# Performance work log

Measured on AMD Instinct MI355X. Metric: run time of the kernel, lower is better.

## Reference

```python
import jax, jax.numpy as jnp
import numpy as np

B, C, H, W = 4, 256, 64, 64
C8 = C // 8

def setup_inputs() -> dict:
    key = jax.random.key(0)
    ks = jax.random.split(key, 9)
    s_in = 1.0 / np.sqrt(C)
    return {
        "feat1": jax.random.normal(ks[0], (B, C, H, W), jnp.float32),
        "feat2": jax.random.normal(ks[1], (B, C, H, W), jnp.float32),
        # 1x1 conv weights stored as [out_ch, in_ch]
        "Wq": jax.random.normal(ks[2], (C8, C), jnp.float32) * s_in,
        "bq": jax.random.normal(ks[3], (C8,), jnp.float32) * s_in,
        "Wk": jax.random.normal(ks[4], (C8, C), jnp.float32) * s_in,
        "bk": jax.random.normal(ks[5], (C8,), jnp.float32) * s_in,
        "Wv": jax.random.normal(ks[6], (C, C), jnp.float32) * s_in,
        "bv": jax.random.normal(ks[7], (C,), jnp.float32) * s_in,
        "gamma": jax.random.normal(ks[8], (1,), jnp.float32) * 0.1,
    }

def reference(feat1, feat2, Wq, bq, Wk, bk, Wv, bv, gamma):
    b, c, h, w = feat1.shape
    n = h * w
    f1 = feat1.reshape(b, c, n)  # [B,C,N]
    f2 = feat2.reshape(b, c, n)
    # 1x1 convs == per-pixel channel matmuls
    q = jnp.einsum("oc,bcn->bno", Wq, f1) + bq            # [B,N,C8]
    k = jnp.einsum("oc,bcn->bon", Wk, f2) + bk[None, :, None]  # [B,C8,N]
    v = jnp.einsum("oc,bcn->bon", Wv, f2) + bv[None, :, None]  # [B,C,N]
    energy = jnp.einsum("bno,bom->bnm", q, k)             # [B,N,N] (unscaled)
    attn = jax.nn.softmax(energy, axis=-1)
    # out[b,c,m] = sum_n v[b,c,n] * attn[b,m,n]
    out = jnp.einsum("bcn,bmn->bcm", v, attn).reshape(b, c, h, w)
    return gamma * out + feat1
```

## Files before the change

### kernel.cpp

```cpp
#include <hip/hip_runtime.h>
#include <hip/hip_bf16.h>
#include <stdint.h>

typedef __attribute__((ext_vector_type(8))) short bf16x8;
typedef __attribute__((ext_vector_type(4))) short short4v;
typedef __attribute__((ext_vector_type(4))) float f32x4;
typedef __attribute__((ext_vector_type(16))) float f32x16;
typedef __attribute__((ext_vector_type(4))) unsigned uint4v;

#define LDS3(p) ((__attribute__((address_space(3))) void*)(p))
#define GLB1(p) ((const __attribute__((address_space(1))) void*)(p))

constexpr int Bc = 4;
constexpr int Cc = 256;
constexpr int Nn = 4096;
constexpr int Dq = 32;
constexpr float L2E = 1.4426950408889634f;

__device__ __forceinline__ short f2b(float x) {
  union { float f; uint32_t u; } v; v.f = x;
  uint32_t r = (v.u + 0x7fffu + ((v.u >> 16) & 1u)) >> 16;
  return (short)(r & 0xffffu);
}
__device__ __forceinline__ float b2f(short s) {
  union { uint32_t u; float f; } v; v.u = ((uint32_t)(uint16_t)s) << 16;
  return v.f;
}
__device__ __forceinline__ unsigned fb(float x) {
  union { float f; unsigned u; } v; v.f = x; return v.u;
}

__global__ __launch_bounds__(256) void prep_transpose(
    const float* __restrict__ f1, const float* __restrict__ f2,
    short* __restrict__ f1T, short* __restrict__ f2T) {
  __shared__ float tile[64][65];
  const int bx = blockIdx.x;
  const int which = bx >> 10;
  const int rem = bx & 1023;
  const int b = rem >> 8;
  const int cb = (rem >> 6) & 3;
  const int nb = rem & 63;
  const float* src = which ? f2 : f1;
  short* dst = which ? f2T : f1T;
  const int c0 = cb * 64, n0 = nb * 64;
  const int tid = threadIdx.x;
  const int lane = tid & 63;
  const int row4 = tid >> 6;
#pragma unroll
  for (int i = 0; i < 16; ++i) {
    const int cl = row4 + i * 4;
    tile[cl][lane] = src[(size_t)(b * Cc + c0 + cl) * Nn + n0 + lane];
  }
  __syncthreads();
#pragma unroll
  for (int i = 0; i < 16; ++i) {
    const int nl = row4 + i * 4;
    dst[(size_t)(b * Nn + n0 + nl) * Cc + c0 + lane] = f2b(tile[lane][nl]);
  }
}

__global__ __launch_bounds__(256) void prep_weights(
    const float* __restrict__ Wq, const float* __restrict__ Wk,
    const float* __restrict__ Wv, short* __restrict__ Wq_b,
    short* __restrict__ Wk_b, short* __restrict__ Wv_b) {
  const int base = (blockIdx.x * 256 + threadIdx.x) * 4;
#pragma unroll
  for (int j = 0; j < 4; ++j) {
    const int idx = base + j;
    if (idx < 8192) Wq_b[idx] = f2b(Wq[idx]);
    else if (idx < 16384) Wk_b[idx - 8192] = f2b(Wk[idx - 8192]);
    else if (idx < 16384 + 65536) Wv_b[idx - 16384] = f2b(Wv[idx - 16384]);
  }
}

__global__ __launch_bounds__(256) void proj_qkv(
    const short* __restrict__ f1T, const short* __restrict__ f2T,
    const short* __restrict__ Wq_b, const float* __restrict__ bq,
    const short* __restrict__ Wk_b, const float* __restrict__ bk,
    const short* __restrict__ Wv_b, const float* __restrict__ bv,
    short* __restrict__ q_ws, short* __restrict__ k_ws,
    short* __restrict__ v_ws) {
  const int bx = blockIdx.x;
  const int b = bx >> 6;
  const int n0 = (bx & 63) * 64;
  const int tid = threadIdx.x;
  const int w = tid >> 6;
  const int lane = tid & 63;
  const int l16 = lane & 15;
  const int g = lane >> 4;

#pragma unroll
  for (int qk = 0; qk < 2; ++qk) {
    const short* X = qk ? f2T : f1T;
    const short* Wm = qk ? Wk_b : Wq_b;
    const float* bias_p = qk ? bk : bq;
    short* outp = qk ? k_ws : q_ws;
    f32x4 accq[2] = {(f32x4){0.f, 0.f, 0.f, 0.f}, (f32x4){0.f, 0.f, 0.f, 0.f}};
#pragma unroll
    for (int kc = 0; kc < 8; ++kc) {
      const bf16x8 a = *(const bf16x8*)&X[(size_t)(b * Nn + n0 + w * 16 + l16) * Cc + kc * 32 + g * 8];
#pragma unroll
      for (int ob = 0; ob < 2; ++ob) {
        const bf16x8 bb = *(const bf16x8*)&Wm[(ob * 16 + l16) * Cc + kc * 32 + g * 8];
        accq[ob] = __builtin_amdgcn_mfma_f32_16x16x32_bf16(a, bb, accq[ob], 0, 0, 0);
      }
    }
#pragma unroll
    for (int ob = 0; ob < 2; ++ob) {
      const float bias = bias_p[ob * 16 + l16];
#pragma unroll
      for (int r = 0; r < 4; ++r) {
        const int n = n0 + w * 16 + g * 4 + r;
        outp[(size_t)(b * Nn + n) * Dq + ob * 16 + l16] = f2b(accq[ob][r] + bias);
      }
    }
  }

  {
    f32x4 acc[4][4];
#pragma unroll
    for (int ci = 0; ci < 4; ++ci)
#pragma unroll
      for (int nb = 0; nb < 4; ++nb) acc[ci][nb] = (f32x4){0.f, 0.f, 0.f, 0.f};
#pragma unroll
    for (int kc = 0; kc < 8; ++kc) {
      bf16x8 bfr[4];
#pragma unroll
      for (int nb = 0; nb < 4; ++nb)
        bfr[nb] = *(const bf16x8*)&f2T[(size_t)(b * Nn + n0 + nb * 16 + l16) * Cc + kc * 32 + g * 8];
#pragma unroll
      for (int ci = 0; ci < 4; ++ci) {
        const bf16x8 afr = *(const bf16x8*)&Wv_b[((w * 4 + ci) * 16 + l16) * Cc + kc * 32 + g * 8];
#pragma unroll
        for (int nb = 0; nb < 4; ++nb)
          acc[ci][nb] = __builtin_amdgcn_mfma_f32_16x16x32_bf16(afr, bfr[nb], acc[ci][nb], 0, 0, 0);
      }
    }
#pragma unroll
    for (int ci = 0; ci < 4; ++ci) {
#pragma unroll
      for (int r = 0; r < 4; ++r) {
        const int c = (w * 4 + ci) * 16 + g * 4 + r;
        const float bias = bv[c];
#pragma unroll
        for (int nb = 0; nb < 4; ++nb) {
          const int n = n0 + nb * 16 + l16;
          v_ws[(size_t)(b * Cc + c) * Nn + n] = f2b(acc[ci][nb][r] + bias);
        }
      }
    }
  }
}

constexpr int NT = 64;
constexpr int VBUF = 256 * NT * 2;
constexpr int SBYTES = 2 * VBUF;

template <int KS>
__global__ __launch_bounds__(256, 2) void attn_kernel(
    const short* __restrict__ q_ws, const short* __restrict__ k_ws,
    const short* __restrict__ v_ws, short* __restrict__ Opart,
    float* __restrict__ mlm, short* __restrict__ mll) {
  constexpr int KSPAN = Nn / KS;
  constexpr int NTILES = KSPAN / NT;
  __shared__ __align__(16) char smem[SBYTES];
  const int bx = blockIdx.x;
  const int swz = (bx & 7) * (16 * KS) + (bx >> 3);
  const int ks = swz >> 7;
  const int rem = swz & 127;
  const int b = rem >> 5;
  const int m0 = (rem & 31) * 128;
  const int n0 = ks * KSPAN;
  const int tid = threadIdx.x;
  const int w = tid >> 6;
  const int lane = tid & 63;
  const int l31 = lane & 31;
  const int h = lane >> 5;

  const short* qbase = q_ws + (size_t)(b * Nn + m0 + w * 32 + l31) * Dq + h * 8;
  const bf16x8 qf0 = *(const bf16x8*)(qbase);
  const bf16x8 qf1 = *(const bf16x8*)(qbase + 16);

  const int kswap = (l31 & 0x13) | ((l31 & 4) << 1) | ((l31 & 8) >> 1);
  const short* kptr = k_ws + (size_t)(b * Nn + n0 + kswap) * Dq + h * 8;

  const int cth = tid >> 3;
  const int c7 = cth & 7;
  const int koff = 8 * ((tid & 7) ^ c7);
  const short* vsrc[8];
#pragma unroll
  for (int j = 0; j < 8; ++j)
    vsrc[j] = v_ws + (size_t)(b * Cc + j * 32 + cth) * Nn + n0 + koff;

  f32x16 acc[8] = {};
  float mrun = -INFINITY, lrun = 0.f;

#pragma unroll
  for (int j = 0; j < 8; ++j) {
    char* ldst = &smem[(j * 256 + tid) * 16];
    __builtin_amdgcn_global_load_lds(GLB1(vsrc[j]), LDS3(ldst), 16, 0, 0);
    vsrc[j] += NT;
  }
  bf16x8 kf[4];
#pragma unroll
  for (int nb = 0; nb < 2; ++nb)
#pragma unroll
    for (int s = 0; s < 2; ++s)
      kf[nb * 2 + s] = *(const bf16x8*)(kptr + nb * 32 * Dq + s * 16);
  kptr += NT * Dq;

  const f32x16 Z = {};
  for (int t = 0; t < NTILES; ++t) {
    const int buf = t & 1;
    f32x16 sa[2];
    sa[0] = __builtin_amdgcn_mfma_f32_32x32x16_bf16(kf[0], qf0, Z, 0, 0, 0);
    sa[0] = __builtin_amdgcn_mfma_f32_32x32x16_bf16(kf[1], qf1, sa[0], 0, 0, 0);
    sa[1] = __builtin_amdgcn_mfma_f32_32x32x16_bf16(kf[2], qf0, Z, 0, 0, 0);
    sa[1] = __builtin_amdgcn_mfma_f32_32x32x16_bf16(kf[3], qf1, sa[1], 0, 0, 0);

    float tmax = sa[0][0];
#pragma unroll
    for (int r = 1; r < 16; ++r) tmax = fmaxf(tmax, sa[0][r]);
#pragma unroll
    for (int r = 0; r < 16; ++r) tmax = fmaxf(tmax, sa[1][r]);
    tmax = fmaxf(tmax, __shfl_xor(tmax, 32));
    if (__any(tmax > mrun + 8.f)) {
      const float mnew = fmaxf(mrun, tmax);
      const float scl = exp2f((mrun - mnew) * L2E);
      float sv[16];
#pragma unroll
      for (int r = 0; r < 16; ++r)
        sv[r] = __shfl(scl, (r & 3) + 8 * (r >> 2) + 4 * h);
#pragma unroll
      for (int cb = 0; cb < 8; ++cb)
#pragma unroll
        for (int r = 0; r < 16; ++r) acc[cb][r] *= sv[r];
      lrun *= scl;
      mrun = mnew;
    }
    const float nml = -mrun * L2E;
    float psum = 0.f;
    unsigned pu[16];
#pragma unroll
    for (int nb = 0; nb < 2; ++nb)
#pragma unroll
      for (int q = 0; q < 8; ++q) {
        const float p0 = exp2f(fmaf(sa[nb][2 * q], L2E, nml));
        const float p1 = exp2f(fmaf(sa[nb][2 * q + 1], L2E, nml));
        psum += p0 + p1;
        pu[nb * 8 + q] = __builtin_amdgcn_perm(fb(p1), fb(p0), 0x07060302u);
      }
    psum += __shfl_xor(psum, 32);
    lrun += psum;

    asm volatile("s_waitcnt vmcnt(0)" ::: "memory");
    __syncthreads();

    if (t + 1 < NTILES) {
#pragma unroll
      for (int j = 0; j < 8; ++j) {
        char* ldst = &smem[(buf ^ 1) * VBUF + (j * 256 + tid) * 16];
        __builtin_amdgcn_global_load_lds(GLB1(vsrc[j]), LDS3(ldst), 16, 0, 0);
        vsrc[j] += NT;
      }
#pragma unroll
      for (int nb = 0; nb < 2; ++nb)
#pragma unroll
        for (int s = 0; s < 2; ++s)
          kf[nb * 2 + s] = *(const bf16x8*)(kptr + nb * 32 * Dq + s * 16);
      kptr += NT * Dq;
    }

    const int sb = buf * VBUF;
#pragma unroll
    for (int f = 0; f < 4; ++f) {
      const uint4v au = {pu[4 * f], pu[4 * f + 1], pu[4 * f + 2], pu[4 * f + 3]};
      const bf16x8 A = __builtin_bit_cast(bf16x8, au);
      const char* vbase =
          &smem[sb + l31 * 128 + ((((f << 1) + h) ^ (l31 & 7)) << 4)];
#pragma unroll
      for (int cb = 0; cb < 8; ++cb) {
        const bf16x8 vB = *(const bf16x8*)(vbase + cb * 4096);
        acc[cb] = __builtin_amdgcn_mfma_f32_32x32x16_bf16(A, vB, acc[cb], 0, 0, 0);
      }
    }
  }

  __syncthreads();
  if (h == 0) {
    const int m = m0 + w * 32 + l31;
    mlm[(size_t)(ks * Bc + b) * Nn + m] = mrun;
    mll[(size_t)(ks * Bc + b) * Nn + m] = f2b(lrun);
  }
  char* strip = smem + w * 10240;
#pragma unroll
  for (int ph = 0; ph < 2; ++ph) {
#pragma unroll
    for (int cb2 = 0; cb2 < 4; ++cb2) {
      const int cb = ph * 4 + cb2;
      const int cs = cb2 * 32 + l31;
#pragma unroll
      for (int q = 0; q < 8; ++q) {
        const int mloc = ((2 * q) & 3) + 8 * (q >> 1) + 4 * h;
        const unsigned pv = __builtin_amdgcn_perm(
            fb(acc[cb][2 * q + 1]), fb(acc[cb][2 * q]), 0x07060302u);
        *(unsigned*)(strip + cs * 80 + mloc * 2) = pv;
      }
    }
    asm volatile("s_waitcnt lgkmcnt(0)" ::: "memory");
#pragma unroll
    for (int i = 0; i < 8; ++i) {
      const int gi = i * 64 + lane;
      const int cs = gi >> 2, gq = gi & 3;
      const uint4v vv = *(const uint4v*)(strip + cs * 80 + gq * 16);
      const int cg = ph * 128 + cs;
      const size_t off =
          ((size_t)(ks * Bc + b) * Cc + cg) * Nn + m0 + w * 32 + gq * 8;
      *(uint4v*)&Opart[off] = vv;
    }
    asm volatile("s_waitcnt lgkmcnt(0)" ::: "memory");
  }
}

template <int KS>
__global__ __launch_bounds__(256) void combine_kernel(
    const short* __restrict__ Opart, const float* __restrict__ mlm,
    const short* __restrict__ mll, const float* __restrict__ feat1,
    const float* __restrict__ gamma_p, float* __restrict__ out) {
  __shared__ float aLDS[KS][64];
  const int bx = blockIdx.x;
  const int b = bx >> 6;
  const int m0 = (bx & 63) * 64;
  const int tid = threadIdx.x;
  if (tid < 64) {
    const int m = m0 + tid;
    float mm[KS], ll[KS], ms = -INFINITY;
#pragma unroll
    for (int ks = 0; ks < KS; ++ks) {
      mm[ks] = mlm[(size_t)(ks * Bc + b) * Nn + m];
      ll[ks] = b2f(mll[(size_t)(ks * Bc + b) * Nn + m]);
      ms = fmaxf(ms, mm[ks]);
    }
    float es[KS], lsum = 0.f;
#pragma unroll
    for (int ks = 0; ks < KS; ++ks) {
      es[ks] = exp2f((mm[ks] - ms) * L2E);
      lsum += ll[ks] * es[ks];
    }
    const float inv = 1.f / lsum;
#pragma unroll
    for (int ks = 0; ks < KS; ++ks) aLDS[ks][tid] = es[ks] * inv;
  }
  __syncthreads();
  const int mg = tid & 7;
  const int cb = tid >> 3;
  float aks[KS][8];
#pragma unroll
  for (int ks = 0; ks < KS; ++ks)
#pragma unroll
    for (int j = 0; j < 8; ++j) aks[ks][j] = aLDS[ks][mg * 8 + j];
  const float gam = gamma_p[0];
#pragma unroll 2
  for (int i = 0; i < 8; ++i) {
    const int c = cb + i * 32;
    float v[8] = {0.f, 0.f, 0.f, 0.f, 0.f, 0.f, 0.f, 0.f};
#pragma unroll
    for (int ks = 0; ks < KS; ++ks) {
      const bf16x8 ov = *(const bf16x8*)
          &Opart[((size_t)(ks * Bc + b) * Cc + c) * Nn + m0 + mg * 8];
#pragma unroll
      for (int j = 0; j < 8; ++j) v[j] += b2f(ov[j]) * aks[ks][j];
    }
    const size_t base = ((size_t)(b * Cc + c)) * Nn + m0 + mg * 8;
    const f32x4 fa = *(const f32x4*)&feat1[base];
    const f32x4 fbv = *(const f32x4*)&feat1[base + 4];
    f32x4 o0, o1;
#pragma unroll
    for (int j = 0; j < 4; ++j) {
      o0[j] = gam * v[j] + fa[j];
      o1[j] = gam * v[4 + j] + fbv[j];
    }
    *(f32x4*)&out[base] = o0;
    *(f32x4*)&out[base + 4] = o1;
  }
}

extern "C" void kernel_launch(void* const* d_in, const int* in_sizes, int n_in,
                              void* d_out, int out_size, void* d_ws,
                              size_t ws_size, hipStream_t stream) {
  const float* feat1 = (const float*)d_in[0];
  const float* feat2 = (const float*)d_in[1];
  const float* Wq = (const float*)d_in[2];
  const float* bq = (const float*)d_in[3];
  const float* Wk = (const float*)d_in[4];
  const float* bk = (const float*)d_in[5];
  const float* Wv = (const float*)d_in[6];
  const float* bv = (const float*)d_in[7];
  const float* gamma = (const float*)d_in[8];
  float* out = (float*)d_out;
  char* ws = (char*)d_ws;

  const size_t need4 = 44433408;
  if (ws_size >= need4) {
    short* Opart = (short*)(ws + 0);
    short* f1T  = (short*)(ws + 0);
    short* f2T  = (short*)(ws + 8388608);
    short* Wq_b = (short*)(ws + 16777216);
    short* Wk_b = (short*)(ws + 16793600);
    short* Wv_b = (short*)(ws + 16809984);
    short* q_ws = (short*)(ws + 33554432);
    short* k_ws = (short*)(ws + 34603008);
    short* v_ws = (short*)(ws + 35651584);
    float* mlm  = (float*)(ws + 44040192);
    short* mll  = (short*)(ws + 44302336);

    prep_transpose<<<2048, 256, 0, stream>>>(feat1, feat2, f1T, f2T);
    prep_weights<<<80, 256, 0, stream>>>(Wq, Wk, Wv, Wq_b, Wk_b, Wv_b);
    proj_qkv<<<256, 256, 0, stream>>>(f1T, f2T, Wq_b, bq, Wk_b, bk, Wv_b, bv,
                                      q_ws, k_ws, v_ws);
    attn_kernel<4><<<512, 256, 0, stream>>>(q_ws, k_ws, v_ws, Opart, mlm, mll);
    combine_kernel<4><<<256, 256, 0, stream>>>(Opart, mlm, mll, feat1, gamma,
                                               out);
  } else {
    short* Opart = (short*)(ws + 0);
    short* f1T  = (short*)(ws + 0);
    short* f2T  = (short*)(ws + 8388608);
    short* Wq_b = (short*)(ws + 16777216);
    short* Wk_b = (short*)(ws + 16793600);
    short* Wv_b = (short*)(ws + 16809984);
    short* q_ws = (short*)(ws + 16941056);
    short* k_ws = (short*)(ws + 17989632);
    short* v_ws = (short*)(ws + 19038208);
    float* mlm  = (float*)(ws + 27426816);
    short* mll  = (short*)(ws + 27557888);

    prep_transpose<<<2048, 256, 0, stream>>>(feat1, feat2, f1T, f2T);
    prep_weights<<<80, 256, 0, stream>>>(Wq, Wk, Wv, Wq_b, Wk_b, Wv_b);
    proj_qkv<<<256, 256, 0, stream>>>(f1T, f2T, Wq_b, bq, Wk_b, bk, Wv_b, bv,
                                      q_ws, k_ws, v_ws);
    attn_kernel<2><<<256, 256, 0, stream>>>(q_ws, k_ws, v_ws, Opart, mlm, mll);
    combine_kernel<2><<<256, 256, 0, stream>>>(Opart, mlm, mll, feat1, gamma,
                                               out);
  }
}
```

Measured before the change: 102.6 us.

## Software-pipeline attention: compute next tile's softmax while current PV MFMAs run

Shrinks the key tile from 64 to 32 and restructures the flash-attention loop so that the QK scores and softmax probabilities for tile t+1 are computed before the PV MFMAs for tile t, with a prologue for the first tile. Deferred rescaling of the accumulators, s_setprio around the MFMA block, and tree reductions for max/sum are added. The V LDS staging layout and the epilogue strip sizes are adjusted to the smaller tile. The aim is to overlap exp/VALU work with matrix-core work and to halve LDS use for occupancy, at the cost of more barriers per key span and extra register pressure.

```diff
diff --git a/kernel.cpp b/kernel.cpp
--- a/kernel.cpp
+++ b/kernel.cpp
@@ -152,7 +152,7 @@
   }
 }
 
-constexpr int NT = 64;
+constexpr int NT = 32;
 constexpr int VBUF = 256 * NT * 2;
 constexpr int SBYTES = 2 * VBUF;
 
@@ -184,105 +184,150 @@
   const int kswap = (l31 & 0x13) | ((l31 & 4) << 1) | ((l31 & 8) >> 1);
   const short* kptr = k_ws + (size_t)(b * Nn + n0 + kswap) * Dq + h * 8;
 
-  const int cth = tid >> 3;
-  const int c7 = cth & 7;
-  const int koff = 8 * ((tid & 7) ^ c7);
-  const short* vsrc[8];
-#pragma unroll
-  for (int j = 0; j < 8; ++j)
-    vsrc[j] = v_ws + (size_t)(b * Cc + j * 32 + cth) * Nn + n0 + koff;
+  const int cth = tid >> 2;
+  const int koff = 8 * ((tid & 3) ^ (cth & 3));
+  const short* vsrc[4];
+#pragma unroll
+  for (int j = 0; j < 4; ++j)
+    vsrc[j] = v_ws + (size_t)(b * Cc + j * 64 + cth) * Nn + n0 + koff;
 
   f32x16 acc[8] = {};
   float mrun = -INFINITY, lrun = 0.f;
 
 #pragma unroll
-  for (int j = 0; j < 8; ++j) {
+  for (int j = 0; j < 4; ++j) {
     char* ldst = &smem[(j * 256 + tid) * 16];
     __builtin_amdgcn_global_load_lds(GLB1(vsrc[j]), LDS3(ldst), 16, 0, 0);
     vsrc[j] += NT;
   }
-  bf16x8 kf[4];
-#pragma unroll
-  for (int nb = 0; nb < 2; ++nb)
-#pragma unroll
-    for (int s = 0; s < 2; ++s)
-      kf[nb * 2 + s] = *(const bf16x8*)(kptr + nb * 32 * Dq + s * 16);
+  bf16x8 kfa = *(const bf16x8*)(kptr);
+  bf16x8 kfb = *(const bf16x8*)(kptr + 16);
   kptr += NT * Dq;
+  asm volatile("s_waitcnt vmcnt(0)" ::: "memory");
+  __syncthreads();
 
   const f32x16 Z = {};
+  unsigned puC[8], puN[8];
+
+  {
+    f32x16 sa = __builtin_amdgcn_mfma_f32_32x32x16_bf16(kfa, qf0, Z, 0, 0, 0);
+    sa = __builtin_amdgcn_mfma_f32_32x32x16_bf16(kfb, qf1, sa, 0, 0, 0);
+    kfa = *(const bf16x8*)(kptr);
+    kfb = *(const bf16x8*)(kptr + 16);
+    kptr += NT * Dq;
+    float t8[8], t4[4];
+#pragma unroll
+    for (int i = 0; i < 8; ++i) t8[i] = fmaxf(sa[i], sa[i + 8]);
+#pragma unroll
+    for (int i = 0; i < 4; ++i) t4[i] = fmaxf(t8[i], t8[i + 4]);
+    float tmax = fmaxf(fmaxf(t4[0], t4[2]), fmaxf(t4[1], t4[3]));
+    tmax = fmaxf(tmax, __shfl_xor(tmax, 32));
+    mrun = tmax;
+    const float nml = -mrun * L2E;
+    float p[16];
+#pragma unroll
+    for (int r = 0; r < 16; ++r) p[r] = exp2f(fmaf(sa[r], L2E, nml));
+#pragma unroll
+    for (int q = 0; q < 8; ++q)
+      puC[q] = __builtin_amdgcn_perm(fb(p[2 * q + 1]), fb(p[2 * q]), 0x07060302u);
+    float s8[8], s4[4];
+#pragma unroll
+    for (int i = 0; i < 8; ++i) s8[i] = p[i] + p[i + 8];
+#pragma unroll
+    for (int i = 0; i < 4; ++i) s4[i] = s8[i] + s8[i + 4];
+    float psum = (s4[0] + s4[2]) + (s4[1] + s4[3]);
+    psum += __shfl_xor(psum, 32);
+    lrun = psum;
+  }
+#pragma unroll
+  for (int j = 0; j < 4; ++j) {
+    char* ldst = &smem[VBUF + (j * 256 + tid) * 16];
+    __builtin_amdgcn_global_load_lds(GLB1(vsrc[j]), LDS3(ldst), 16, 0, 0);
+    vsrc[j] += NT;
+  }
+
+#pragma unroll 2
   for (int t = 0; t < NTILES; ++t) {
     const int buf = t & 1;
-    f32x16 sa[2];
-    sa[0] = __builtin_amdgcn_mfma_f32_32x32x16_bf16(kf[0], qf0, Z, 0, 0, 0);
-    sa[0] = __builtin_amdgcn_mfma_f32_32x32x16_bf16(kf[1], qf1, sa[0], 0, 0, 0);
-    sa[1] = __builtin_amdgcn_mfma_f32_32x32x16_bf16(kf[2], qf0, Z, 0, 0, 0);
-    sa[1] = __builtin_amdgcn_mfma_f32_32x32x16_bf16(kf[3], qf1, sa[1], 0, 0, 0);
-
-    float tmax = sa[0][0];
-#pragma unroll
-    for (int r = 1; r < 16; ++r) tmax = fmaxf(tmax, sa[0][r]);
-#pragma unroll
-    for (int r = 0; r < 16; ++r) tmax = fmaxf(tmax, sa[1][r]);
-    tmax = fmaxf(tmax, __shfl_xor(tmax, 32));
-    if (__any(tmax > mrun + 8.f)) {
-      const float mnew = fmaxf(mrun, tmax);
-      const float scl = exp2f((mrun - mnew) * L2E);
-      float sv[16];
-#pragma unroll
-      for (int r = 0; r < 16; ++r)
-        sv[r] = __shfl(scl, (r & 3) + 8 * (r >> 2) + 4 * h);
-#pragma unroll
-      for (int cb = 0; cb < 8; ++cb)
-#pragma unroll
-        for (int r = 0; r < 16; ++r) acc[cb][r] *= sv[r];
-      lrun *= scl;
-      mrun = mnew;
-    }
-    const float nml = -mrun * L2E;
-    float psum = 0.f;
-    unsigned pu[16];
-#pragma unroll
-    for (int nb = 0; nb < 2; ++nb)
-#pragma unroll
-      for (int q = 0; q < 8; ++q) {
-        const float p0 = exp2f(fmaf(sa[nb][2 * q], L2E, nml));
-        const float p1 = exp2f(fmaf(sa[nb][2 * q + 1], L2E, nml));
-        psum += p0 + p1;
-        pu[nb * 8 + q] = __builtin_amdgcn_perm(fb(p1), fb(p0), 0x07060302u);
-      }
-    psum += __shfl_xor(psum, 32);
-    lrun += psum;
-
-    asm volatile("s_waitcnt vmcnt(0)" ::: "memory");
-    __syncthreads();
-
+    bool resc = false;
+    float sv[16];
     if (t + 1 < NTILES) {
-#pragma unroll
-      for (int j = 0; j < 8; ++j) {
-        char* ldst = &smem[(buf ^ 1) * VBUF + (j * 256 + tid) * 16];
-        __builtin_amdgcn_global_load_lds(GLB1(vsrc[j]), LDS3(ldst), 16, 0, 0);
-        vsrc[j] += NT;
-      }
-#pragma unroll
-      for (int nb = 0; nb < 2; ++nb)
-#pragma unroll
-        for (int s = 0; s < 2; ++s)
-          kf[nb * 2 + s] = *(const bf16x8*)(kptr + nb * 32 * Dq + s * 16);
-      kptr += NT * Dq;
-    }
-
+      f32x16 sa = __builtin_amdgcn_mfma_f32_32x32x16_bf16(kfa, qf0, Z, 0, 0, 0);
+      sa = __builtin_amdgcn_mfma_f32_32x32x16_bf16(kfb, qf1, sa, 0, 0, 0);
+      if (t + 2 < NTILES) {
+        kfa = *(const bf16x8*)(kptr);
+        kfb = *(const bf16x8*)(kptr + 16);
+        kptr += NT * Dq;
+      }
+      float t8[8], t4[4];
+#pragma unroll
+      for (int i = 0; i < 8; ++i) t8[i] = fmaxf(sa[i], sa[i + 8]);
+#pragma unroll
+      for (int i = 0; i < 4; ++i) t4[i] = fmaxf(t8[i], t8[i + 4]);
+      float tmax = fmaxf(fmaxf(t4[0], t4[2]), fmaxf(t4[1], t4[3]));
+      tmax = fmaxf(tmax, __shfl_xor(tmax, 32));
+      resc = __any(tmax > mrun + 8.f);
+      if (resc) {
+        const float mnew = fmaxf(mrun, tmax);
+        const float scl = exp2f((mrun - mnew) * L2E);
+#pragma unroll
+        for (int r = 0; r < 16; ++r)
+          sv[r] = __shfl(scl, (r & 3) + 8 * (r >> 2) + 4 * h);
+        lrun *= scl;
+        mrun = mnew;
+      }
+      const float nml = -mrun * L2E;
+      float p[16];
+#pragma unroll
+      for (int r = 0; r < 16; ++r) p[r] = exp2f(fmaf(sa[r], L2E, nml));
+#pragma unroll
+      for (int q = 0; q < 8; ++q)
+        puN[q] = __builtin_amdgcn_perm(fb(p[2 * q + 1]), fb(p[2 * q]), 0x07060302u);
+      float s8[8], s4[4];
+#pragma unroll
+      for (int i = 0; i < 8; ++i) s8[i] = p[i] + p[i + 8];
+#pragma unroll
+      for (int i = 0; i < 4; ++i) s4[i] = s8[i] + s8[i + 4];
+      float psum = (s4[0] + s4[2]) + (s4[1] + s4[3]);
+      psum += __shfl_xor(psum, 32);
+      lrun += psum;
+    }
+
+    __builtin_amdgcn_s_setprio(1);
     const int sb = buf * VBUF;
 #pragma unroll
-    for (int f = 0; f < 4; ++f) {
-      const uint4v au = {pu[4 * f], pu[4 * f + 1], pu[4 * f + 2], pu[4 * f + 3]};
+    for (int f = 0; f < 2; ++f) {
+      const uint4v au = {puC[4 * f], puC[4 * f + 1], puC[4 * f + 2], puC[4 * f + 3]};
       const bf16x8 A = __builtin_bit_cast(bf16x8, au);
       const char* vbase =
-          &smem[sb + l31 * 128 + ((((f << 1) + h) ^ (l31 & 7)) << 4)];
+          &smem[sb + l31 * 64 + ((((f << 1) + h) ^ (l31 & 3)) << 4)];
 #pragma unroll
       for (int cb = 0; cb < 8; ++cb) {
-        const bf16x8 vB = *(const bf16x8*)(vbase + cb * 4096);
+        const bf16x8 vB = *(const bf16x8*)(vbase + cb * 2048);
         acc[cb] = __builtin_amdgcn_mfma_f32_32x32x16_bf16(A, vB, acc[cb], 0, 0, 0);
       }
+    }
+    __builtin_amdgcn_s_setprio(0);
+
+    if (t + 1 < NTILES) {
+      if (resc) {
+#pragma unroll
+        for (int cb = 0; cb < 8; ++cb)
+#pragma unroll
+          for (int r = 0; r < 16; ++r) acc[cb][r] *= sv[r];
+      }
+      asm volatile("s_waitcnt vmcnt(0)" ::: "memory");
+      __syncthreads();
+      if (t + 2 < NTILES) {
+#pragma unroll
+        for (int j = 0; j < 4; ++j) {
+          char* ldst = &smem[buf * VBUF + (j * 256 + tid) * 16];
+          __builtin_amdgcn_global_load_lds(GLB1(vsrc[j]), LDS3(ldst), 16, 0, 0);
+          vsrc[j] += NT;
+        }
+      }
+#pragma unroll
+      for (int q = 0; q < 8; ++q) puC[q] = puN[q];
     }
   }
 
@@ -292,12 +337,12 @@
     mlm[(size_t)(ks * Bc + b) * Nn + m] = mrun;
     mll[(size_t)(ks * Bc + b) * Nn + m] = f2b(lrun);
   }
-  char* strip = smem + w * 10240;
-#pragma unroll
-  for (int ph = 0; ph < 2; ++ph) {
-#pragma unroll
-    for (int cb2 = 0; cb2 < 4; ++cb2) {
-      const int cb = ph * 4 + cb2;
+  char* strip = smem + w * 5120;
+#pragma unroll
+  for (int ph = 0; ph < 4; ++ph) {
+#pragma unroll
+    for (int cb2 = 0; cb2 < 2; ++cb2) {
+      const int cb = ph * 2 + cb2;
       const int cs = cb2 * 32 + l31;
 #pragma unroll
       for (int q = 0; q < 8; ++q) {
@@ -309,11 +354,11 @@
     }
     asm volatile("s_waitcnt lgkmcnt(0)" ::: "memory");
 #pragma unroll
-    for (int i = 0; i < 8; ++i) {
+    for (int i = 0; i < 4; ++i) {
       const int gi = i * 64 + lane;
       const int cs = gi >> 2, gq = gi & 3;
       const uint4v vv = *(const uint4v*)(strip + cs * 80 + gq * 16);
-      const int cg = ph * 128 + cs;
+      const int cg = ph * 64 + cs;
       const size_t off =
           ((size_t)(ks * Bc + b) * Cc + cg) * Nn + m0 + w * 32 + gq * 8;
       *(uint4v*)&Opart[off] = vv;
```

New measurement: 112.3 us. 1.09x slower.

## Fuse feature transpose into projection kernel and tree-reduce softmax max/sum

Applied to the files above, without the earlier changes.

Removes the separate prep_transpose kernel. The projection kernel now reads fp32 features directly, transposes and converts them to bf16 in shared memory, and feeds the MFMAs from LDS. This avoids writing and re-reading the transposed bf16 copies in global memory and saves one launch. The attention loop also replaces the serial max and sum chains with tree reductions and raises wave priority around the PV MFMA block. The fused kernel adds about 50KB of LDS and several block barriers, which may reduce occupancy across its 256 blocks.

```diff
diff --git a/kernel.cpp b/kernel.cpp
--- a/kernel.cpp
+++ b/kernel.cpp
@@ -30,35 +30,6 @@
   union { float f; unsigned u; } v; v.f = x; return v.u;
 }
 
-__global__ __launch_bounds__(256) void prep_transpose(
-    const float* __restrict__ f1, const float* __restrict__ f2,
-    short* __restrict__ f1T, short* __restrict__ f2T) {
-  __shared__ float tile[64][65];
-  const int bx = blockIdx.x;
-  const int which = bx >> 10;
-  const int rem = bx & 1023;
-  const int b = rem >> 8;
-  const int cb = (rem >> 6) & 3;
-  const int nb = rem & 63;
-  const float* src = which ? f2 : f1;
-  short* dst = which ? f2T : f1T;
-  const int c0 = cb * 64, n0 = nb * 64;
-  const int tid = threadIdx.x;
-  const int lane = tid & 63;
-  const int row4 = tid >> 6;
-#pragma unroll
-  for (int i = 0; i < 16; ++i) {
-    const int cl = row4 + i * 4;
-    tile[cl][lane] = src[(size_t)(b * Cc + c0 + cl) * Nn + n0 + lane];
-  }
-  __syncthreads();
-#pragma unroll
-  for (int i = 0; i < 16; ++i) {
-    const int nl = row4 + i * 4;
-    dst[(size_t)(b * Nn + n0 + nl) * Cc + c0 + lane] = f2b(tile[lane][nl]);
-  }
-}
-
 __global__ __launch_bounds__(256) void prep_weights(
     const float* __restrict__ Wq, const float* __restrict__ Wk,
     const float* __restrict__ Wv, short* __restrict__ Wq_b,
@@ -73,13 +44,15 @@
   }
 }
 
-__global__ __launch_bounds__(256) void proj_qkv(
-    const short* __restrict__ f1T, const short* __restrict__ f2T,
+__global__ __launch_bounds__(256) void proj_fused(
+    const float* __restrict__ f1, const float* __restrict__ f2,
     const short* __restrict__ Wq_b, const float* __restrict__ bq,
     const short* __restrict__ Wk_b, const float* __restrict__ bk,
     const short* __restrict__ Wv_b, const float* __restrict__ bv,
     short* __restrict__ q_ws, short* __restrict__ k_ws,
     short* __restrict__ v_ws) {
+  __shared__ float ftile[64][65];
+  __shared__ short T[64][264];
   const int bx = blockIdx.x;
   const int b = bx >> 6;
   const int n0 = (bx & 63) * 64;
@@ -88,17 +61,36 @@
   const int lane = tid & 63;
   const int l16 = lane & 15;
   const int g = lane >> 4;
-
-#pragma unroll
-  for (int qk = 0; qk < 2; ++qk) {
-    const short* X = qk ? f2T : f1T;
-    const short* Wm = qk ? Wk_b : Wq_b;
-    const float* bias_p = qk ? bk : bq;
-    short* outp = qk ? k_ws : q_ws;
+  const int lane64 = tid & 63;
+  const int row4 = tid >> 6;
+
+  auto build = [&](const float* __restrict__ src) {
+#pragma unroll
+    for (int cc = 0; cc < 4; ++cc) {
+      __syncthreads();
+#pragma unroll
+      for (int i = 0; i < 16; ++i) {
+        const int cl = row4 + i * 4;
+        ftile[cl][lane64] =
+            src[(size_t)(b * Cc + cc * 64 + cl) * Nn + n0 + lane64];
+      }
+      __syncthreads();
+#pragma unroll
+      for (int i = 0; i < 16; ++i) {
+        const int nl = row4 + i * 4;
+        T[nl][cc * 64 + lane64] = f2b(ftile[lane64][nl]);
+      }
+    }
+    __syncthreads();
+  };
+
+  auto qk_phase = [&](const short* __restrict__ Wm,
+                      const float* __restrict__ bias_p,
+                      short* __restrict__ outp) {
     f32x4 accq[2] = {(f32x4){0.f, 0.f, 0.f, 0.f}, (f32x4){0.f, 0.f, 0.f, 0.f}};
 #pragma unroll
     for (int kc = 0; kc < 8; ++kc) {
-      const bf16x8 a = *(const bf16x8*)&X[(size_t)(b * Nn + n0 + w * 16 + l16) * Cc + kc * 32 + g * 8];
+      const bf16x8 a = *(const bf16x8*)&T[w * 16 + l16][kc * 32 + g * 8];
 #pragma unroll
       for (int ob = 0; ob < 2; ++ob) {
         const bf16x8 bb = *(const bf16x8*)&Wm[(ob * 16 + l16) * Cc + kc * 32 + g * 8];
@@ -114,8 +106,14 @@
         outp[(size_t)(b * Nn + n) * Dq + ob * 16 + l16] = f2b(accq[ob][r] + bias);
       }
     }
-  }
-
+  };
+
+  build(f1);
+  qk_phase(Wq_b, bq, q_ws);
+  __syncthreads();
+
+  build(f2);
+  qk_phase(Wk_b, bk, k_ws);
   {
     f32x4 acc[4][4];
 #pragma unroll
@@ -127,7 +125,7 @@
       bf16x8 bfr[4];
 #pragma unroll
       for (int nb = 0; nb < 4; ++nb)
-        bfr[nb] = *(const bf16x8*)&f2T[(size_t)(b * Nn + n0 + nb * 16 + l16) * Cc + kc * 32 + g * 8];
+        bfr[nb] = *(const bf16x8*)&T[nb * 16 + l16][kc * 32 + g * 8];
 #pragma unroll
       for (int ci = 0; ci < 4; ++ci) {
         const bf16x8 afr = *(const bf16x8*)&Wv_b[((w * 4 + ci) * 16 + l16) * Cc + kc * 32 + g * 8];
@@ -218,11 +216,15 @@
     sa[1] = __builtin_amdgcn_mfma_f32_32x32x16_bf16(kf[2], qf0, Z, 0, 0, 0);
     sa[1] = __builtin_amdgcn_mfma_f32_32x32x16_bf16(kf[3], qf1, sa[1], 0, 0, 0);
 
-    float tmax = sa[0][0];
-#pragma unroll
-    for (int r = 1; r < 16; ++r) tmax = fmaxf(tmax, sa[0][r]);
-#pragma unroll
-    for (int r = 0; r < 16; ++r) tmax = fmaxf(tmax, sa[1][r]);
+    float m16[8];
+#pragma unroll
+    for (int i = 0; i < 8; ++i)
+      m16[i] = fmaxf(fmaxf(sa[0][i], sa[0][i + 8]),
+                     fmaxf(sa[1][i], sa[1][i + 8]));
+    float m3a = fmaxf(fmaxf(m16[0], m16[1]), m16[2]);
+    float m3b = fmaxf(fmaxf(m16[3], m16[4]), m16[5]);
+    float m3c = fmaxf(m16[6], m16[7]);
+    float tmax = fmaxf(fmaxf(m3a, m3b), m3c);
     tmax = fmaxf(tmax, __shfl_xor(tmax, 32));
     if (__any(tmax > mrun + 8.f)) {
       const float mnew = fmaxf(mrun, tmax);
@@ -241,16 +243,25 @@
     const float nml = -mrun * L2E;
     float psum = 0.f;
     unsigned pu[16];
-#pragma unroll
-    for (int nb = 0; nb < 2; ++nb)
-#pragma unroll
-      for (int q = 0; q < 8; ++q) {
-        const float p0 = exp2f(fmaf(sa[nb][2 * q], L2E, nml));
-        const float p1 = exp2f(fmaf(sa[nb][2 * q + 1], L2E, nml));
-        psum += p0 + p1;
-        pu[nb * 8 + q] = __builtin_amdgcn_perm(fb(p1), fb(p0), 0x07060302u);
-      }
-    psum += __shfl_xor(psum, 32);
+    {
+      float p[32];
+#pragma unroll
+      for (int nb = 0; nb < 2; ++nb)
+#pragma unroll
+        for (int r = 0; r < 16; ++r)
+          p[nb * 16 + r] = exp2f(fmaf(sa[nb][r], L2E, nml));
+#pragma unroll
+      for (int q = 0; q < 16; ++q)
+        pu[q] = __builtin_amdgcn_perm(fb(p[2 * q + 1]), fb(p[2 * q]), 0x07060302u);
+      float s8[8];
+#pragma unroll
+      for (int i = 0; i < 8; ++i)
+        s8[i] = (p[i] + p[i + 8]) + (p[i + 16] + p[i + 24]);
+      float s4a = (s8[0] + s8[1]) + (s8[2] + s8[3]);
+      float s4b = (s8[4] + s8[5]) + (s8[6] + s8[7]);
+      psum = s4a + s4b;
+      psum += __shfl_xor(psum, 32);
+    }
     lrun += psum;
 
     asm volatile("s_waitcnt vmcnt(0)" ::: "memory");
@@ -272,6 +283,7 @@
     }
 
     const int sb = buf * VBUF;
+    __builtin_amdgcn_s_setprio(1);
 #pragma unroll
     for (int f = 0; f < 4; ++f) {
       const uint4v au = {pu[4 * f], pu[4 * f + 1], pu[4 * f + 2], pu[4 * f + 3]};
@@ -284,6 +296,7 @@
         acc[cb] = __builtin_amdgcn_mfma_f32_32x32x16_bf16(A, vB, acc[cb], 0, 0, 0);
       }
     }
+    __builtin_amdgcn_s_setprio(0);
   }
 
   __syncthreads();
@@ -403,8 +416,6 @@
   const size_t need4 = 44433408;
   if (ws_size >= need4) {
     short* Opart = (short*)(ws + 0);
-    short* f1T  = (short*)(ws + 0);
-    short* f2T  = (short*)(ws + 8388608);
     short* Wq_b = (short*)(ws + 16777216);
     short* Wk_b = (short*)(ws + 16793600);
     short* Wv_b = (short*)(ws + 16809984);
@@ -414,17 +425,14 @@
     float* mlm  = (float*)(ws + 44040192);
     short* mll  = (short*)(ws + 44302336);
 
-    prep_transpose<<<2048, 256, 0, stream>>>(feat1, feat2, f1T, f2T);
     prep_weights<<<80, 256, 0, stream>>>(Wq, Wk, Wv, Wq_b, Wk_b, Wv_b);
-    proj_qkv<<<256, 256, 0, stream>>>(f1T, f2T, Wq_b, bq, Wk_b, bk, Wv_b, bv,
-                                      q_ws, k_ws, v_ws);
+    proj_fused<<<256, 256, 0, stream>>>(feat1, feat2, Wq_b, bq, Wk_b, bk,
+                                        Wv_b, bv, q_ws, k_ws, v_ws);
     attn_kernel<4><<<512, 256, 0, stream>>>(q_ws, k_ws, v_ws, Opart, mlm, mll);
     combine_kernel<4><<<256, 256, 0, stream>>>(Opart, mlm, mll, feat1, gamma,
                                                out);
   } else {
     short* Opart = (short*)(ws + 0);
-    short* f1T  = (short*)(ws + 0);
-    short* f2T  = (short*)(ws + 8388608);
     short* Wq_b = (short*)(ws + 16777216);
     short* Wk_b = (short*)(ws + 16793600);
     short* Wv_b = (short*)(ws + 16809984);
@@ -434,10 +442,9 @@
     float* mlm  = (float*)(ws + 27426816);
     short* mll  = (short*)(ws + 27557888);
 
-    prep_transpose<<<2048, 256, 0, stream>>>(feat1, feat2, f1T, f2T);
     prep_weights<<<80, 256, 0, stream>>>(Wq, Wk, Wv, Wq_b, Wk_b, Wv_b);
-    proj_qkv<<<256, 256, 0, stream>>>(f1T, f2T, Wq_b, bq, Wk_b, bk, Wv_b, bv,
-                                      q_ws, k_ws, v_ws);
+    proj_fused<<<256, 256, 0, stream>>>(feat1, feat2, Wq_b, bq, Wk_b, bk,
+                                        Wv_b, bv, q_ws, k_ws, v_ws);
     attn_kernel<2><<<256, 256, 0, stream>>>(q_ws, k_ws, v_ws, Opart, mlm, mll);
     combine_kernel<2><<<256, 256, 0, stream>>>(Opart, mlm, mll, feat1, gamma,
                                                out);
```

After: 96.36 us. 6.1% less time.
